# Kernel tuning notes

Measured on AMD Instinct MI355X. Metric: run time of the kernel, lower is better.

## Reference

```python
import jax, jax.numpy as jnp
import numpy as np

DEPTH, E, H, S, V, B = 6, 1024, 16, 2048, 32000, 2
HD = E // H
EPS = 1e-5


def _layernorm(x, w, b):
    mu = jnp.mean(x, axis=-1, keepdims=True)
    var = jnp.mean(jnp.square(x - mu), axis=-1, keepdims=True)
    return (x - mu) * jax.lax.rsqrt(var + EPS) * w + b


def setup_inputs() -> dict:
    key = jax.random.key(0)
    ks = jax.random.split(key, 8)
    std = 0.02
    return {
        "idx": jax.random.randint(ks[0], (B, S), 0, V),
        "tok_emb": jax.random.normal(ks[1], (V, E), jnp.float32) * std,
        "pos_emb": jax.random.normal(ks[2], (S, E), jnp.float32) * std,
        "qkv_w": jax.random.normal(ks[3], (DEPTH, 3 * E, E), jnp.float32) * std,
        "qkv_b": jnp.zeros((DEPTH, 3 * E), jnp.float32),
        "ln1_w": jnp.ones((DEPTH, E), jnp.float32),
        "ln1_b": jnp.zeros((DEPTH, E), jnp.float32),
        "ln2_w": jnp.ones((DEPTH, E), jnp.float32),
        "ln2_b": jnp.zeros((DEPTH, E), jnp.float32),
        "ff1_w": jax.random.normal(ks[4], (DEPTH, 4 * E, E), jnp.float32) * std,
        "ff1_b": jnp.zeros((DEPTH, 4 * E), jnp.float32),
        "ff2_w": jax.random.normal(ks[5], (DEPTH, E, 4 * E), jnp.float32) * std,
        "ff2_b": jnp.zeros((DEPTH, E), jnp.float32),
        "fin_w": jnp.ones((E,), jnp.float32),
        "fin_b": jnp.zeros((E,), jnp.float32),
        "proj_w": jax.random.normal(ks[6], (V, E), jnp.float32) * std,
    }


def _block(x, qkv_w, qkv_b, ln1_w, ln1_b, ln2_w, ln2_b, ff1_w, ff1_b, ff2_w, ff2_b):
    bs, seq, _ = x.shape
    # --- causal MSA (dropout in eval mode -> identity) ---
    xn = _layernorm(x, ln1_w, ln1_b)
    qkv = xn @ qkv_w.T + qkv_b                      # [B,S,3E]
    qkv = qkv.reshape(bs, seq, 3, H, HD)
    q, k, v = (jnp.moveaxis(qkv[:, :, i], 1, 2) for i in range(3))  # [B,H,S,HD]
    scores = jnp.einsum("bhqd,bhkd->bhqk", q, k) / jnp.sqrt(jnp.float32(HD))
    causal = jnp.triu(jnp.ones((seq, seq), bool), k=1)
    scores = jnp.where(causal[None, None], -jnp.inf, scores)
    probs = jax.nn.softmax(scores, axis=-1)
    attn = jnp.einsum("bhqk,bhkd->bqhd", probs, v).reshape(bs, seq, E)
    x = x + attn
    # --- feedforward ---
    xn = _layernorm(x, ln2_w, ln2_b)
    h = jax.nn.gelu(xn @ ff1_w.T + ff1_b, approximate=False)
    x = x + (h @ ff2_w.T + ff2_b)
    return x


def reference(idx, tok_emb, pos_emb, qkv_w, qkv_b, ln1_w, ln1_b, ln2_w, ln2_b,
              ff1_w, ff1_b, ff2_w, ff2_b, fin_w, fin_b, proj_w):
    bs, seq = idx.shape
    x = tok_emb[idx] + pos_emb[jnp.arange(seq)][None]  # [B,S,E]
    for l in range(DEPTH):
        x = _block(x, qkv_w[l], qkv_b[l], ln1_w[l], ln1_b[l], ln2_w[l], ln2_b[l],
                   ff1_w[l], ff1_b[l], ff2_w[l], ff2_b[l])
    x = _layernorm(x, fin_w, fin_b)
    logits = x @ proj_w.T  # [B,S,V], final_proj has no bias
    return logits
```

## Files before the change

### kernel.cpp

```cpp
#include <hip/hip_runtime.h>
#include <hip/hip_bf16.h>

#define DEPTH 6
#define E 1024
#define H 16
#define S 2048
#define V 32000
#define BB 2
#define HD 64
#define NTOK (BB * S)

typedef __attribute__((ext_vector_type(8))) short bf16x8;
typedef __attribute__((ext_vector_type(4))) float f32x4;
typedef unsigned short us;

__device__ inline us f2bf(float f) {
    union { float f; unsigned u; } v; v.f = f;
    unsigned r = v.u + 0x7fff + ((v.u >> 16) & 1);
    return (us)(r >> 16);
}
__device__ inline float bf2f(us b) {
    union { unsigned u; float f; } v; v.u = ((unsigned)b) << 16;
    return v.f;
}

__device__ __forceinline__ void gld16(const us* g, us* l) {
    __builtin_amdgcn_global_load_lds(
        (const __attribute__((address_space(1))) unsigned int*)g,
        (__attribute__((address_space(3))) unsigned int*)l, 16, 0, 0);
}

__global__ __launch_bounds__(256) void cast_kernel(const float* __restrict__ in,
                                                   us* __restrict__ out, int n8) {
    int i = blockIdx.x * 256 + threadIdx.x;
    if (i >= n8) return;
    const float4* p = (const float4*)in + 2 * (size_t)i;
    float4 a = p[0], b = p[1];
    uint4 o;
    o.x = f2bf(a.x) | ((unsigned)f2bf(a.y) << 16);
    o.y = f2bf(a.z) | ((unsigned)f2bf(a.w) << 16);
    o.z = f2bf(b.x) | ((unsigned)f2bf(b.y) << 16);
    o.w = f2bf(b.z) | ((unsigned)f2bf(b.w) << 16);
    ((uint4*)out)[i] = o;
}

__global__ void embed_kernel(const int* __restrict__ idx, const float* __restrict__ tok,
                             const float* __restrict__ pos, float* __restrict__ x) {
    int t = blockIdx.x;
    int s = t & (S - 1);
    int tokid = idx[t];
    int c = threadIdx.x * 4;
    float4 a = *(const float4*)&tok[(size_t)tokid * E + c];
    float4 p = *(const float4*)&pos[(size_t)s * E + c];
    float4 o; o.x = a.x + p.x; o.y = a.y + p.y; o.z = a.z + p.z; o.w = a.w + p.w;
    *(float4*)&x[(size_t)t * E + c] = o;
}

__global__ __launch_bounds__(256) void ln_kernel(const float* __restrict__ x,
                                                 const float* __restrict__ w,
                                                 const float* __restrict__ b,
                                                 us* __restrict__ out) {
    int row = blockIdx.x;
    int tid = threadIdx.x;
    int c = tid * 4;
    float4 v = *(const float4*)&x[(size_t)row * E + c];
    float s  = v.x + v.y + v.z + v.w;
    float sq = v.x * v.x + v.y * v.y + v.z * v.z + v.w * v.w;
    __shared__ float red[8];
    for (int o = 32; o > 0; o >>= 1) { s += __shfl_xor(s, o); sq += __shfl_xor(sq, o); }
    int wave = tid >> 6, lane = tid & 63;
    if (lane == 0) { red[wave] = s; red[4 + wave] = sq; }
    __syncthreads();
    if (tid == 0) {
        red[0] = red[0] + red[1] + red[2] + red[3];
        red[4] = red[4] + red[5] + red[6] + red[7];
    }
    __syncthreads();
    float mean = red[0] * (1.0f / E);
    float var  = red[4] * (1.0f / E) - mean * mean;
    float rstd = rsqrtf(var + 1e-5f);
    float4 wv = *(const float4*)&w[c];
    float4 bv = *(const float4*)&b[c];
    unsigned a0 = f2bf((v.x - mean) * rstd * wv.x + bv.x);
    unsigned a1 = f2bf((v.y - mean) * rstd * wv.y + bv.y);
    unsigned a2 = f2bf((v.z - mean) * rstd * wv.z + bv.z);
    unsigned a3 = f2bf((v.w - mean) * rstd * wv.w + bv.w);
    uint2 o; o.x = a0 | (a1 << 16); o.y = a2 | (a3 << 16);
    *(uint2*)&out[(size_t)row * E + c] = o;
}

#define GPH(dd, fb, STAGE, ISVM, IS12)                                              \
  {                                                                                 \
    bf16x8 afr0[2], afr1[2];                                                        \
    if ((fb) == 0) {                                                                \
      _Pragma("unroll")                                                             \
      for (int n = 0; n < 4; n++)                                                   \
        _Pragma("unroll")                                                           \
        for (int ks = 0; ks < 2; ks++)                                              \
          bfr[n][ks] = *(const bf16x8*)&lds[32768 + (dd) * 16384 +                  \
              (brow + n * 16) * 64 + ((ks * 4 + g4) ^ xg) * 8];                     \
    }                                                                               \
    _Pragma("unroll")                                                               \
    for (int ks = 0; ks < 2; ks++) {                                                \
      afr0[ks] = *(const bf16x8*)&lds[(dd) * 16384 + ((fb) >> 1) * 4096 +           \
          arow0 * 64 + ((ks * 4 + g4) ^ xg) * 8];                                   \
      afr1[ks] = *(const bf16x8*)&lds[(dd) * 16384 + ((fb) >> 1) * 4096 +           \
          arow1 * 64 + ((ks * 4 + g4) ^ xg) * 8];                                   \
    }                                                                               \
    STAGE;                                                                          \
    __builtin_amdgcn_sched_barrier(0);                                              \
    if (IS12) asm volatile("s_waitcnt lgkmcnt(8)" ::: "memory");                    \
    __builtin_amdgcn_s_barrier();                                                   \
    asm volatile("s_waitcnt lgkmcnt(0)" ::: "memory");                              \
    __builtin_amdgcn_sched_barrier(0);                                              \
    __builtin_amdgcn_s_setprio(1);                                                  \
    _Pragma("unroll")                                                               \
    for (int n = 0; n < 4; n++)                                                     \
      _Pragma("unroll")                                                             \
      for (int ks = 0; ks < 2; ks++) {                                              \
        acc[(fb)][n]     = __builtin_amdgcn_mfma_f32_16x16x32_bf16(afr0[ks], bfr[n][ks], acc[(fb)][n], 0, 0, 0);     \
        acc[(fb) + 1][n] = __builtin_amdgcn_mfma_f32_16x16x32_bf16(afr1[ks], bfr[n][ks], acc[(fb) + 1][n], 0, 0, 0); \
      }                                                                             \
    __builtin_amdgcn_s_setprio(0);                                                  \
    __builtin_amdgcn_sched_barrier(0);                                              \
    if (ISVM) asm volatile("s_waitcnt vmcnt(6)" ::: "memory");                      \
    __builtin_amdgcn_s_barrier();                                                   \
  }

template <int OUT_BF16, int ACT_GELU, int HAS_BIAS>
__global__ __launch_bounds__(512, 2) void gemm256(const us* __restrict__ A, int lda,
                                                  const us* __restrict__ Bw, int ldb,
                                                  const float* __restrict__ bias,
                                                  void* __restrict__ outp,
                                                  int M, int N, int K, int ldo) {
    __shared__ us lds[65536];
    int tid = threadIdx.x;
    int nwg = gridDim.x;
    int wgid = blockIdx.x;
    int chunk = nwg >> 3;
    int sw = (wgid & 7) * chunk + (wgid >> 3);
    int MB = M >> 8;
    int bm = (sw % MB) * 256;
    int bn = (sw / MB) * 256;
    int w = tid >> 6, lane = tid & 63;
    int wr = w >> 2, wc = w & 3;
    int l15 = lane & 15, g4 = lane >> 4;
    int xg = l15 & 7;
    int arow0 = (wr ? 32 : 0) + l15;
    int arow1 = arow0 + 16;
    int brow = wc * 64 + l15;
    int NT = K >> 6;

    f32x4 acc[8][4] = {};
    bf16x8 bfr[4][2];

    auto stA = [&](int u, int dd, int h) {
        int uu = (u < NT) ? u : NT - 1;
        #pragma unroll
        for (int i = 0; i < 2; i++) {
            int k = tid + i * 512;
            int q = 2 * h + (k >> 9);
            int r = (k >> 3) & 63;
            int tr = q * 32 + (r & 31) + ((r >> 5) << 7);
            int gp = (k & 7) ^ (r & 7);
            gld16(A + (size_t)(bm + tr) * lda + uu * 64 + gp * 8,
                  &lds[dd * 16384 + h * 8192 + k * 8]);
        }
    };
    auto stB = [&](int u, int dd, int h) {
        int uu = (u < NT) ? u : NT - 1;
        #pragma unroll
        for (int i = 0; i < 2; i++) {
            int k = tid + i * 512;
            int row = h * 128 + (k >> 3);
            int gp = (k & 7) ^ ((k >> 3) & 7);
            gld16(Bw + (size_t)(bn + row) * ldb + uu * 64 + gp * 8,
                  &lds[32768 + dd * 16384 + h * 8192 + k * 8]);
        }
    };

    stB(0, 0, 0); stB(0, 0, 1); stA(0, 0, 0); stA(0, 0, 1);
    stB(1, 1, 0); stB(1, 1, 1); stA(1, 1, 0);
    __builtin_amdgcn_sched_barrier(0);
    asm volatile("s_waitcnt vmcnt(6)" ::: "memory");
    __builtin_amdgcn_s_barrier();

    #pragma unroll 1
    for (int t = 0; t < NT; t += 2) {
        GPH(0, 0, stA(t + 1, 1, 1), 0, 1)
        GPH(0, 2, stB(t + 2, 0, 0), 0, 0)
        GPH(0, 4, stB(t + 2, 0, 1), 0, 0)
        GPH(0, 6, stA(t + 2, 0, 0), 1, 0)
        GPH(1, 0, stA(t + 2, 0, 1), 0, 1)
        GPH(1, 2, stB(t + 3, 1, 0), 0, 0)
        GPH(1, 4, stB(t + 3, 1, 1), 0, 0)
        GPH(1, 6, stA(t + 3, 1, 0), 1, 0)
    }

    float* outf = (float*)outp;
    us* outb = (us*)outp;
    #pragma unroll
    for (int mf = 0; mf < 8; mf++)
        #pragma unroll
        for (int n = 0; n < 4; n++)
            #pragma unroll
            for (int j = 0; j < 4; j++) {
                int r = bm + wr * 128 + mf * 16 + g4 * 4 + j;
                int c = bn + wc * 64 + n * 16 + l15;
                float v = acc[mf][n][j];
                if (HAS_BIAS) v += bias[c];
                if (ACT_GELU) v = 0.5f * v * (1.0f + erff(v * 0.70710678118f));
                if (OUT_BF16) outb[(size_t)r * ldo + c] = f2bf(v);
                else outf[(size_t)r * ldo + c] = v;
            }
}

template <int SPLITK>
__global__ __launch_bounds__(256) void gemm_bf16(const us* __restrict__ A, int lda,
                                                 const us* __restrict__ Bw, int ldb,
                                                 void* __restrict__ outp,
                                                 int M, int N, int K, int ldo) {
    __shared__ us As[2 * 128 * 32];
    __shared__ us Bs[2 * 128 * 32];
    int tid = threadIdx.x;
    int nwg = gridDim.x;
    int chunk = nwg >> 3;
    int wgid = blockIdx.x;
    int sw = (wgid & 7) * chunk + (wgid >> 3);

    int bm, bn;
    us* outb = (us*)outp;
    {
        int kz = sw >> 8;
        int rem = sw & 255;
        bm = (rem & 31) * 128;
        bn = (rem >> 5) * 128;
        A  += (size_t)kz * K;
        Bw += (size_t)kz * K;
        outb += (size_t)kz * M * ldo;
    }

    int wave = tid >> 6, lane = tid & 63;
    int wr = wave >> 1, wc = wave & 1;
    int l15 = lane & 15, g4 = lane >> 4;
    f32x4 acc[4][4] = {};

    for (int k0 = 0; k0 < K; k0 += 64) {
        #pragma unroll
        for (int p4 = 0; p4 < 4; p4++) {
            int p = p4 * 256 + tid;
            int ks = p >> 9, q = p & 511;
            int row = q >> 2, c8 = (q & 3) * 8;
            gld16(&A[(size_t)(bm + row) * lda + k0 + ks * 32 + c8], &As[p * 8]);
            gld16(&Bw[(size_t)(bn + row) * ldb + k0 + ks * 32 + c8], &Bs[p * 8]);
        }
        __syncthreads();
        bf16x8 a[4][2], bfr[4][2];
        #pragma unroll
        for (int m = 0; m < 4; m++)
            #pragma unroll
            for (int ks = 0; ks < 2; ks++)
                a[m][ks] = *(const bf16x8*)&As[ks * 4096 + (wr * 64 + m * 16 + l15) * 32 + g4 * 8];
        #pragma unroll
        for (int n = 0; n < 4; n++)
            #pragma unroll
            for (int ks = 0; ks < 2; ks++)
                bfr[n][ks] = *(const bf16x8*)&Bs[ks * 4096 + (wc * 64 + n * 16 + l15) * 32 + g4 * 8];
        #pragma unroll
        for (int m = 0; m < 4; m++)
            #pragma unroll
            for (int n = 0; n < 4; n++)
                #pragma unroll
                for (int ks = 0; ks < 2; ks++)
                    acc[m][n] = __builtin_amdgcn_mfma_f32_16x16x32_bf16(a[m][ks], bfr[n][ks], acc[m][n], 0, 0, 0);
        __syncthreads();
    }

    #pragma unroll
    for (int m = 0; m < 4; m++)
        #pragma unroll
        for (int n = 0; n < 4; n++)
            #pragma unroll
            for (int j = 0; j < 4; j++) {
                int r = bm + wr * 64 + m * 16 + g4 * 4 + j;
                int c = bn + wc * 64 + n * 16 + l15;
                outb[(size_t)r * ldo + c] = f2bf(acc[m][n][j]);
            }
}

__global__ __launch_bounds__(256) void combine_ff2(const us* __restrict__ p0,
                                                   const us* __restrict__ p1,
                                                   const float* __restrict__ bias,
                                                   float* __restrict__ x) {
    int g = blockIdx.x * 256 + threadIdx.x;
    size_t base = (size_t)g * 8;
    int col = (int)(base & (E - 1));
    uint4 a = *(const uint4*)&p0[base];
    uint4 b = *(const uint4*)&p1[base];
    const us* pa = (const us*)&a;
    const us* pb = (const us*)&b;
    float4 x0 = *(const float4*)&x[base];
    float4 x1 = *(const float4*)&x[base + 4];
    float4 w0 = *(const float4*)&bias[col];
    float4 w1 = *(const float4*)&bias[col + 4];
    x0.x += bf2f(pa[0]) + bf2f(pb[0]) + w0.x;
    x0.y += bf2f(pa[1]) + bf2f(pb[1]) + w0.y;
    x0.z += bf2f(pa[2]) + bf2f(pb[2]) + w0.z;
    x0.w += bf2f(pa[3]) + bf2f(pb[3]) + w0.w;
    x1.x += bf2f(pa[4]) + bf2f(pb[4]) + w1.x;
    x1.y += bf2f(pa[5]) + bf2f(pb[5]) + w1.y;
    x1.z += bf2f(pa[6]) + bf2f(pb[6]) + w1.z;
    x1.w += bf2f(pa[7]) + bf2f(pb[7]) + w1.w;
    *(float4*)&x[base] = x0;
    *(float4*)&x[base + 4] = x1;
}

__global__ __launch_bounds__(256) void transpose_v(const us* __restrict__ qkv,
                                                   us* __restrict__ vT) {
    int kt = blockIdx.x, h = blockIdx.y, b = blockIdx.z;
    int tid = threadIdx.x;
    __shared__ us T[64][72];
    const size_t base = (size_t)b * S * 3072 + 2048 + h * 64;
    int k0 = kt * 64;
    #pragma unroll
    for (int it = 0; it < 2; it++) {
        int p = tid + it * 256;
        int key = p & 63, c8 = (p >> 6) * 8;
        uint4 v = *(const uint4*)&qkv[base + (size_t)(k0 + key) * 3072 + c8];
        us* pv = (us*)&v;
        #pragma unroll
        for (int e = 0; e < 8; e++) T[c8 + e][key] = pv[e];
    }
    __syncthreads();
    const size_t obase = ((size_t)(b * H + h) * 64) * S + k0;
    #pragma unroll
    for (int it = 0; it < 2; it++) {
        int o = tid + it * 256;
        int d = o >> 3, cc = (o & 7) * 8;
        uint4 v = *(const uint4*)&T[d][cc];
        *(uint4*)&vT[obase + (size_t)d * S + cc] = v;
    }
}

__global__ __launch_bounds__(512, 4) void attn_kernel(const us* __restrict__ qkv,
                                                      const us* __restrict__ vT,
                                                      float* __restrict__ x) {
    int qt = blockIdx.x, h = blockIdx.y, b = blockIdx.z;
    int tid = threadIdx.x;
    int w = tid >> 6, lane = tid & 63;
    int l15 = lane & 15, g4 = lane >> 4;
    int s0 = qt * 128;
    int qrow_base = s0 + w * 16;
    const size_t qbase = (size_t)b * S * 3072;
    const size_t vtbase = ((size_t)(b * H + h) * 64) * S;

    __shared__ us K_lds[2][64 * 64];
    __shared__ us VT_lds[2][64 * 64];
    __shared__ us P_lds[8][16 * 72];

    bf16x8 q[2];
    #pragma unroll
    for (int dc = 0; dc < 2; dc++)
        q[dc] = *(const bf16x8*)&qkv[qbase + (size_t)(qrow_base + l15) * 3072 + h * 64 + dc * 32 + 8 * g4];

    f32x4 O[4] = {};
    float m_run[4], l_run[4];
    #pragma unroll
    for (int j = 0; j < 4; j++) { m_run[j] = -INFINITY; l_run[j] = 0.0f; }

    int lastt = 2 * qt + 1;
    {
        int p = tid, row = p >> 3, cc = p & 7;
        int scc = cc ^ (row & 7);
        gld16(&qkv[qbase + (size_t)(0 + row) * 3072 + 1024 + h * 64 + scc * 8], &K_lds[0][p * 8]);
        gld16(&vT[vtbase + (size_t)row * S + 0 + scc * 8], &VT_lds[0][p * 8]);
    }
    __syncthreads();

    for (int t = 0; t <= lastt; t++) {
        int bb = t & 1;
        if (t < lastt) {
            int p = tid, row = p >> 3, cc = p & 7;
            int scc = cc ^ (row & 7);
            gld16(&qkv[qbase + (size_t)((t + 1) * 64 + row) * 3072 + 1024 + h * 64 + scc * 8], &K_lds[bb ^ 1][p * 8]);
            gld16(&vT[vtbase + (size_t)row * S + (t + 1) * 64 + scc * 8], &VT_lds[bb ^ 1][p * 8]);
        }
        int k0 = t * 64;
        if (k0 <= qrow_base + 15) {
            f32x4 sf[4];
            __builtin_amdgcn_s_setprio(1);
            #pragma unroll
            for (int c = 0; c < 4; c++) {
                f32x4 z = {};
                int row = c * 16 + l15;
                #pragma unroll
                for (int dc = 0; dc < 2; dc++) {
                    int ch = (dc * 4 + g4) ^ (row & 7);
                    bf16x8 kb = *(const bf16x8*)&K_lds[bb][row * 64 + ch * 8];
                    z = __builtin_amdgcn_mfma_f32_16x16x32_bf16(q[dc], kb, z, 0, 0, 0);
                }
                sf[c] = z;
            }
            __builtin_amdgcn_s_setprio(0);
            bool needmask = (k0 + 63 > qrow_base);
            float pr[4][4], alpha[4];
            #pragma unroll
            for (int j = 0; j < 4; j++) {
                int qrow = qrow_base + g4 * 4 + j;
                float v0 = sf[0][j] * 0.125f, v1 = sf[1][j] * 0.125f;
                float v2 = sf[2][j] * 0.125f, v3 = sf[3][j] * 0.125f;
                if (needmask) {
                    if (k0 +      l15 > qrow) v0 = -INFINITY;
                    if (k0 + 16 + l15 > qrow) v1 = -INFINITY;
                    if (k0 + 32 + l15 > qrow) v2 = -INFINITY;
                    if (k0 + 48 + l15 > qrow) v3 = -INFINITY;
                }
                float tm = fmaxf(fmaxf(v0, v1), fmaxf(v2, v3));
                tm = fmaxf(tm, __shfl_xor(tm, 1, 16));
                tm = fmaxf(tm, __shfl_xor(tm, 2, 16));
                tm = fmaxf(tm, __shfl_xor(tm, 4, 16));
                tm = fmaxf(tm, __shfl_xor(tm, 8, 16));
                float mnew = fmaxf(m_run[j], tm);
                float p0 = __expf(v0 - mnew), p1 = __expf(v1 - mnew);
                float p2 = __expf(v2 - mnew), p3 = __expf(v3 - mnew);
                float ts = (p0 + p1) + (p2 + p3);
                ts += __shfl_xor(ts, 1, 16);
                ts += __shfl_xor(ts, 2, 16);
                ts += __shfl_xor(ts, 4, 16);
                ts += __shfl_xor(ts, 8, 16);
                alpha[j] = __expf(m_run[j] - mnew);
                l_run[j] = l_run[j] * alpha[j] + ts;
                m_run[j] = mnew;
                pr[0][j] = p0; pr[1][j] = p1; pr[2][j] = p2; pr[3][j] = p3;
            }
            #pragma unroll
            for (int f = 0; f < 4; f++)
                #pragma unroll
                for (int j = 0; j < 4; j++) O[f][j] *= alpha[j];
            us* Pw = &P_lds[w][0];
            #pragma unroll
            for (int c = 0; c < 4; c++)
                #pragma unroll
                for (int j = 0; j < 4; j++)
                    Pw[(g4 * 4 + j) * 72 + c * 16 + l15] = f2bf(pr[c][j]);
            __builtin_amdgcn_s_setprio(1);
            #pragma unroll
            for (int kc = 0; kc < 2; kc++) {
                bf16x8 pa = *(const bf16x8*)&Pw[l15 * 72 + kc * 32 + g4 * 8];
                #pragma unroll
                for (int dt = 0; dt < 4; dt++) {
                    int row = dt * 16 + l15;
                    int ch = (kc * 4 + g4) ^ (row & 7);
                    bf16x8 vb = *(const bf16x8*)&VT_lds[bb][row * 64 + ch * 8];
                    O[dt] = __builtin_amdgcn_mfma_f32_16x16x32_bf16(pa, vb, O[dt], 0, 0, 0);
                }
            }
            __builtin_amdgcn_s_setprio(0);
        }
        __syncthreads();
    }
    #pragma unroll
    for (int dt = 0; dt < 4; dt++)
        #pragma unroll
        for (int j = 0; j < 4; j++) {
            size_t o = ((size_t)b * S + qrow_base + g4 * 4 + j) * E + h * 64 + dt * 16 + l15;
            x[o] += O[dt][j] / l_run[j];
        }
}

extern "C" void kernel_launch(void* const* d_in, const int* in_sizes, int n_in,
                              void* d_out, int out_size, void* d_ws, size_t ws_size,
                              hipStream_t stream) {
    const int*   idx    = (const int*)d_in[0];
    const float* tok    = (const float*)d_in[1];
    const float* pos    = (const float*)d_in[2];
    const float* qkv_w  = (const float*)d_in[3];
    const float* qkv_b  = (const float*)d_in[4];
    const float* ln1_w  = (const float*)d_in[5];
    const float* ln1_b  = (const float*)d_in[6];
    const float* ln2_w  = (const float*)d_in[7];
    const float* ln2_b  = (const float*)d_in[8];
    const float* ff1_w  = (const float*)d_in[9];
    const float* ff1_b  = (const float*)d_in[10];
    const float* ff2_w  = (const float*)d_in[11];
    const float* ff2_b  = (const float*)d_in[12];
    const float* fin_w  = (const float*)d_in[13];
    const float* fin_b  = (const float*)d_in[14];
    const float* proj_w = (const float*)d_in[15];

    char* ws = (char*)d_ws;
    float* x    = (float*)ws;
    us*    xn   = (us*)(ws + 16777216);
    us*    qkvb = (us*)(ws + 25165824);
    us*    hbuf = (us*)(ws + 50331648);
    us*    wbuf = (us*)(ws + 83886080);
    us*    vTb  = (us*)(ws + 92274688);
    us*    pbuf = qkvb;

    embed_kernel<<<NTOK, 256, 0, stream>>>(idx, tok, pos, x);
    for (int l = 0; l < DEPTH; l++) {
        ln_kernel<<<NTOK, 256, 0, stream>>>(x, ln1_w + l * E, ln1_b + l * E, xn);
        cast_kernel<<<1536, 256, 0, stream>>>(qkv_w + (size_t)l * 3 * E * E, wbuf, 3 * E * E / 8);
        gemm256<1, 0, 1><<<192, 512, 0, stream>>>(
            xn, E, wbuf, E, qkv_b + l * 3 * E, qkvb, NTOK, 3 * E, E, 3 * E);
        transpose_v<<<dim3(S / 64, H, BB), 256, 0, stream>>>(qkvb, vTb);
        attn_kernel<<<dim3(S / 128, H, BB), 512, 0, stream>>>(qkvb, vTb, x);
        ln_kernel<<<NTOK, 256, 0, stream>>>(x, ln2_w + l * E, ln2_b + l * E, xn);
        cast_kernel<<<2048, 256, 0, stream>>>(ff1_w + (size_t)l * 4 * E * E, wbuf, 4 * E * E / 8);
        gemm256<1, 1, 1><<<256, 512, 0, stream>>>(
            xn, E, wbuf, E, ff1_b + l * 4 * E, hbuf, NTOK, 4 * E, E, 4 * E);
        cast_kernel<<<2048, 256, 0, stream>>>(ff2_w + (size_t)l * E * 4 * E, wbuf, 4 * E * E / 8);
        gemm_bf16<1><<<512, 256, 0, stream>>>(
            hbuf, 4 * E, wbuf, 4 * E, qkvb, NTOK, E, 2 * E, E);
        combine_ff2<<<2048, 256, 0, stream>>>(qkvb, qkvb + (size_t)NTOK * E, ff2_b + l * E, x);
    }
    ln_kernel<<<NTOK, 256, 0, stream>>>(x, fin_w, fin_b, xn);
    cast_kernel<<<16000, 256, 0, stream>>>(proj_w, pbuf, V * E / 8);
    gemm256<0, 0, 0><<<2000, 512, 0, stream>>>(
        xn, E, pbuf, E, nullptr, d_out, NTOK, V, E, V);
}
```

Before: 1.982 ms.

## Fuse FF2 split-K combine with next LayerNorm, switch QKV GEMM, prescale Q

Merges the FF2 split-K combine kernel with the following LayerNorm (next layer's LN1, or the final LN), which removes one kernel launch and one full pass over x per layer. The QKV projection moves from the 256-tile gemm256 kernel to a generalized 128-tile gemm_bf16 with a bias epilogue and 768 workgroups, which changes occupancy and grid shape. Q is also multiplied by 1/8 at load time instead of scaling every score. That scaling is exact in bf16 because it is a power of two, so precision is unchanged.

```diff
diff --git a/kernel.cpp b/kernel.cpp
--- a/kernel.cpp
+++ b/kernel.cpp
@@ -87,6 +87,52 @@
     unsigned a3 = f2bf((v.w - mean) * rstd * wv.w + bv.w);
     uint2 o; o.x = a0 | (a1 << 16); o.y = a2 | (a3 << 16);
     *(uint2*)&out[(size_t)row * E + c] = o;
+}
+
+__global__ __launch_bounds__(256) void combine_ln(const us* __restrict__ p0,
+                                                  const us* __restrict__ p1,
+                                                  const float* __restrict__ bias,
+                                                  float* __restrict__ x,
+                                                  const float* __restrict__ w,
+                                                  const float* __restrict__ b,
+                                                  us* __restrict__ out) {
+    int row = blockIdx.x;
+    int tid = threadIdx.x;
+    int c = tid * 4;
+    size_t base = (size_t)row * E + c;
+    float4 v = *(const float4*)&x[base];
+    uint2 a = *(const uint2*)&p0[base];
+    uint2 bb2 = *(const uint2*)&p1[base];
+    float4 bi = *(const float4*)&bias[c];
+    v.x += bf2f((us)(a.x & 0xffff)) + bf2f((us)(bb2.x & 0xffff)) + bi.x;
+    v.y += bf2f((us)(a.x >> 16))    + bf2f((us)(bb2.x >> 16))    + bi.y;
+    v.z += bf2f((us)(a.y & 0xffff)) + bf2f((us)(bb2.y & 0xffff)) + bi.z;
+    v.w += bf2f((us)(a.y >> 16))    + bf2f((us)(bb2.y >> 16))    + bi.w;
+    *(float4*)&x[base] = v;
+
+    float s  = v.x + v.y + v.z + v.w;
+    float sq = v.x * v.x + v.y * v.y + v.z * v.z + v.w * v.w;
+    __shared__ float red[8];
+    for (int o = 32; o > 0; o >>= 1) { s += __shfl_xor(s, o); sq += __shfl_xor(sq, o); }
+    int wave = tid >> 6, lane = tid & 63;
+    if (lane == 0) { red[wave] = s; red[4 + wave] = sq; }
+    __syncthreads();
+    if (tid == 0) {
+        red[0] = red[0] + red[1] + red[2] + red[3];
+        red[4] = red[4] + red[5] + red[6] + red[7];
+    }
+    __syncthreads();
+    float mean = red[0] * (1.0f / E);
+    float var  = red[4] * (1.0f / E) - mean * mean;
+    float rstd = rsqrtf(var + 1e-5f);
+    float4 wv = *(const float4*)&w[c];
+    float4 bv = *(const float4*)&b[c];
+    unsigned a0 = f2bf((v.x - mean) * rstd * wv.x + bv.x);
+    unsigned a1 = f2bf((v.y - mean) * rstd * wv.y + bv.y);
+    unsigned a2 = f2bf((v.z - mean) * rstd * wv.z + bv.z);
+    unsigned a3 = f2bf((v.w - mean) * rstd * wv.w + bv.w);
+    uint2 o; o.x = a0 | (a1 << 16); o.y = a2 | (a3 << 16);
+    *(uint2*)&out[base] = o;
 }
 
 #define GPH(dd, fb, STAGE, ISVM, IS12)                                              \
@@ -215,9 +261,11 @@
             }
 }
 
-template <int SPLITK>
+template <int OUT_BF16, int ACT_GELU, int HAS_BIAS, int HAS_RES, int SPLITK>
 __global__ __launch_bounds__(256) void gemm_bf16(const us* __restrict__ A, int lda,
                                                  const us* __restrict__ Bw, int ldb,
+                                                 const float* __restrict__ bias,
+                                                 const float* __restrict__ res,
                                                  void* __restrict__ outp,
                                                  int M, int N, int K, int ldo) {
     __shared__ us As[2 * 128 * 32];
@@ -230,7 +278,8 @@
 
     int bm, bn;
     us* outb = (us*)outp;
-    {
+    float* outf = (float*)outp;
+    if (SPLITK) {
         int kz = sw >> 8;
         int rem = sw & 255;
         bm = (rem & 31) * 128;
@@ -238,6 +287,10 @@
         A  += (size_t)kz * K;
         Bw += (size_t)kz * K;
         outb += (size_t)kz * M * ldo;
+    } else {
+        int MB = M >> 7;
+        bm = (sw % MB) * 128;
+        bn = (sw / MB) * 128;
     }
 
     int wave = tid >> 6, lane = tid & 63;
@@ -284,35 +337,13 @@
             for (int j = 0; j < 4; j++) {
                 int r = bm + wr * 64 + m * 16 + g4 * 4 + j;
                 int c = bn + wc * 64 + n * 16 + l15;
-                outb[(size_t)r * ldo + c] = f2bf(acc[m][n][j]);
+                float v = acc[m][n][j];
+                if (HAS_BIAS) v += bias[c];
+                if (ACT_GELU) v = 0.5f * v * (1.0f + erff(v * 0.70710678118f));
+                if (HAS_RES) v += res[(size_t)r * ldo + c];
+                if (OUT_BF16) outb[(size_t)r * ldo + c] = f2bf(v);
+                else outf[(size_t)r * ldo + c] = v;
             }
-}
-
-__global__ __launch_bounds__(256) void combine_ff2(const us* __restrict__ p0,
-                                                   const us* __restrict__ p1,
-                                                   const float* __restrict__ bias,
-                                                   float* __restrict__ x) {
-    int g = blockIdx.x * 256 + threadIdx.x;
-    size_t base = (size_t)g * 8;
-    int col = (int)(base & (E - 1));
-    uint4 a = *(const uint4*)&p0[base];
-    uint4 b = *(const uint4*)&p1[base];
-    const us* pa = (const us*)&a;
-    const us* pb = (const us*)&b;
-    float4 x0 = *(const float4*)&x[base];
-    float4 x1 = *(const float4*)&x[base + 4];
-    float4 w0 = *(const float4*)&bias[col];
-    float4 w1 = *(const float4*)&bias[col + 4];
-    x0.x += bf2f(pa[0]) + bf2f(pb[0]) + w0.x;
-    x0.y += bf2f(pa[1]) + bf2f(pb[1]) + w0.y;
-    x0.z += bf2f(pa[2]) + bf2f(pb[2]) + w0.z;
-    x0.w += bf2f(pa[3]) + bf2f(pb[3]) + w0.w;
-    x1.x += bf2f(pa[4]) + bf2f(pb[4]) + w1.x;
-    x1.y += bf2f(pa[5]) + bf2f(pb[5]) + w1.y;
-    x1.z += bf2f(pa[6]) + bf2f(pb[6]) + w1.z;
-    x1.w += bf2f(pa[7]) + bf2f(pb[7]) + w1.w;
-    *(float4*)&x[base] = x0;
-    *(float4*)&x[base + 4] = x1;
 }
 
 __global__ __launch_bounds__(256) void transpose_v(const us* __restrict__ qkv,
@@ -360,8 +391,12 @@
 
     bf16x8 q[2];
     #pragma unroll
-    for (int dc = 0; dc < 2; dc++)
+    for (int dc = 0; dc < 2; dc++) {
         q[dc] = *(const bf16x8*)&qkv[qbase + (size_t)(qrow_base + l15) * 3072 + h * 64 + dc * 32 + 8 * g4];
+        us* qq = (us*)&q[dc];
+        #pragma unroll
+        for (int e = 0; e < 8; e++) qq[e] = f2bf(bf2f(qq[e]) * 0.125f);
+    }
 
     f32x4 O[4] = {};
     float m_run[4], l_run[4];
@@ -407,8 +442,8 @@
             #pragma unroll
             for (int j = 0; j < 4; j++) {
                 int qrow = qrow_base + g4 * 4 + j;
-                float v0 = sf[0][j] * 0.125f, v1 = sf[1][j] * 0.125f;
-                float v2 = sf[2][j] * 0.125f, v3 = sf[3][j] * 0.125f;
+                float v0 = sf[0][j], v1 = sf[1][j];
+                float v2 = sf[2][j], v3 = sf[3][j];
                 if (needmask) {
                     if (k0 +      l15 > qrow) v0 = -INFINITY;
                     if (k0 + 16 + l15 > qrow) v1 = -INFINITY;
@@ -498,11 +533,11 @@
     us*    pbuf = qkvb;
 
     embed_kernel<<<NTOK, 256, 0, stream>>>(idx, tok, pos, x);
+    ln_kernel<<<NTOK, 256, 0, stream>>>(x, ln1_w, ln1_b, xn);
     for (int l = 0; l < DEPTH; l++) {
-        ln_kernel<<<NTOK, 256, 0, stream>>>(x, ln1_w + l * E, ln1_b + l * E, xn);
         cast_kernel<<<1536, 256, 0, stream>>>(qkv_w + (size_t)l * 3 * E * E, wbuf, 3 * E * E / 8);
-        gemm256<1, 0, 1><<<192, 512, 0, stream>>>(
-            xn, E, wbuf, E, qkv_b + l * 3 * E, qkvb, NTOK, 3 * E, E, 3 * E);
+        gemm_bf16<1, 0, 1, 0, 0><<<768, 256, 0, stream>>>(
+            xn, E, wbuf, E, qkv_b + l * 3 * E, nullptr, qkvb, NTOK, 3 * E, E, 3 * E);
         transpose_v<<<dim3(S / 64, H, BB), 256, 0, stream>>>(qkvb, vTb);
         attn_kernel<<<dim3(S / 128, H, BB), 512, 0, stream>>>(qkvb, vTb, x);
         ln_kernel<<<NTOK, 256, 0, stream>>>(x, ln2_w + l * E, ln2_b + l * E, xn);
@@ -510,11 +545,13 @@
         gemm256<1, 1, 1><<<256, 512, 0, stream>>>(
             xn, E, wbuf, E, ff1_b + l * 4 * E, hbuf, NTOK, 4 * E, E, 4 * E);
         cast_kernel<<<2048, 256, 0, stream>>>(ff2_w + (size_t)l * E * 4 * E, wbuf, 4 * E * E / 8);
-        gemm_bf16<1><<<512, 256, 0, stream>>>(
-            hbuf, 4 * E, wbuf, 4 * E, qkvb, NTOK, E, 2 * E, E);
-        combine_ff2<<<2048, 256, 0, stream>>>(qkvb, qkvb + (size_t)NTOK * E, ff2_b + l * E, x);
-    }
-    ln_kernel<<<NTOK, 256, 0, stream>>>(x, fin_w, fin_b, xn);
+        gemm_bf16<1, 0, 0, 0, 1><<<512, 256, 0, stream>>>(
+            hbuf, 4 * E, wbuf, 4 * E, nullptr, nullptr, qkvb, NTOK, E, 2 * E, E);
+        const float* nw = (l < DEPTH - 1) ? (ln1_w + (l + 1) * E) : fin_w;
+        const float* nb = (l < DEPTH - 1) ? (ln1_b + (l + 1) * E) : fin_b;
+        combine_ln<<<NTOK, 256, 0, stream>>>(qkvb, qkvb + (size_t)NTOK * E, ff2_b + l * E,
+                                             x, nw, nb, xn);
+    }
     cast_kernel<<<16000, 256, 0, stream>>>(proj_w, pbuf, V * E / 8);
     gemm256<0, 0, 0><<<2000, 512, 0, stream>>>(
         xn, E, pbuf, E, nullptr, d_out, NTOK, V, E, V);
```

After: 1.973 ms. Within noise of the previous version (-0.4%).
